# Kernel optimization log

Measured on AMD Instinct MI355X. Metric: run time of the kernel, lower is better.

The kernel has to match this reference:

```python
import jax, jax.numpy as jnp
import numpy as np
from functools import partial

K = 5
SCALE = 50000.0
OUT_CHN = 128
IN_CHN = 128
KS = 3

def setup_inputs() -> dict:
    key = jax.random.key(0)
    k1, k2, k3, k4, k5 = jax.random.split(key, 5)
    x = jax.random.normal(k1, (64, IN_CHN, 56, 56), dtype=jnp.float32)
    # xavier_normal-ish init for M and Z
    fan = IN_CHN * KS * KS + OUT_CHN * KS * KS
    std = float(np.sqrt(2.0 / fan))
    M = jax.random.normal(k2, (OUT_CHN, IN_CHN, KS, KS), dtype=jnp.float32) * std
    Z = jax.random.normal(k3, (K, OUT_CHN, IN_CHN, KS, KS), dtype=jnp.float32) * std
    Alpha = jax.random.uniform(k4, (OUT_CHN, 1, 1), dtype=jnp.float32)
    # rv ~ Normal(0, 1/sqrt(scale)), shape (1, K)
    rv = jax.random.normal(k5, (1, K), dtype=jnp.float32) / jnp.sqrt(jnp.float32(SCALE))
    return {"x": x, "M": M, "Z": Z, "Alpha": Alpha, "rv": rv}

def reference(x, M, Z, Alpha, rv):
    # --- SDP stochastic weight generation with pre-normalization ---
    m = M.reshape(-1)                      # (N,)
    z = Z.reshape(K, -1)                   # (K, N)
    A = m * m + jnp.sum(z * z, axis=0) / SCALE
    inv = jax.lax.rsqrt(A)
    m = m * inv
    z = z * inv
    w = (rv @ z)[0] + m                    # (N,)
    real_weights = w.reshape(OUT_CHN, IN_CHN, KS, KS)
    # --- binarize weights and activations ---
    bw = jnp.sign(real_weights)
    ba = jnp.sign(x)
    # --- conv2d, stride 1, padding 1, NCHW/OIHW ---
    out = jax.lax.conv_general_dilated(
        ba, bw, window_strides=(1, 1), padding=((1, 1), (1, 1)),
        dimension_numbers=("NCHW", "OIHW", "NCHW"))
    # per-output-channel scale Alpha (out,1,1) broadcasts over H,W
    out = out * Alpha[None]
    return out
```

## Files before the change

### kernel.cpp

```cpp
#include <hip/hip_runtime.h>
#include <stdint.h>

#define KK 5
#define SCALE_F 50000.0f
#define OC 128
#define IC 128
#define HH 56
#define WW 56
#define NB 64
#define HWSZ (HH * WW)
#define NTAP 9
#define NWEL (OC * IC * NTAP)

#define PD 58
#define NICQ 8

#define PW 60
#define PROWS 58
#define PLANE (PROWS * PW)
#define PLSTRIDE (NB * PLANE)
#define OCPB 2
#define WPT 4

typedef int v4i  __attribute__((ext_vector_type(4)));
typedef int v16i __attribute__((ext_vector_type(16)));

__device__ __forceinline__ constexpr int koff2(int kk) {
    int icb = kk / 9, tap = kk % 9;
    int dh = tap / 3 - 1, dw = tap % 3 - 1;
    return (dh * NICQ + icb * 2) * PD + dw;
}


__global__ void __launch_bounds__(256) border_kernel(int8_t* __restrict__ apk8) {
    int j = blockIdx.x * 256 + threadIdx.x;
    int n  = j / 1824;
    int rj = j - n * 1824;
    int hh, icq, ww;
    if (rj < 928) {
        hh = (rj / 464) * 57;
        int q = rj % 464;
        icq = q / PD;
        ww  = q - icq * PD;
    } else {
        int q = rj - 928;
        hh = 1 + (q >> 4);
        int r2 = q & 15;
        icq = r2 >> 1;
        ww  = (r2 & 1) * 57;
    }
    size_t chunk = (((size_t)n * PD + hh) * NICQ + icq) * PD + ww;
    *(int4*)(apk8 + chunk * 16) = make_int4(0, 0, 0, 0);
}

__global__ void __launch_bounds__(256) wpack_kernel(
    const float* __restrict__ M, const float* __restrict__ Z,
    const float* __restrict__ rv, int8_t* __restrict__ bfrag) {
    int i = blockIdx.x * 256 + threadIdx.x;
    int oc = i / 1152;
    int r1 = i - oc * 1152;
    int ic = r1 / 9;
    int tap = r1 - ic * 9;

    float m  = M[i];
    float z0 = Z[0 * NWEL + i];
    float z1 = Z[1 * NWEL + i];
    float z2 = Z[2 * NWEL + i];
    float z3 = Z[3 * NWEL + i];
    float z4 = Z[4 * NWEL + i];
    float s  = z0 * z0 + z1 * z1 + z2 * z2 + z3 * z3 + z4 * z4;
    float A  = m * m + s * (1.0f / SCALE_F);
    float inv = 1.0f / sqrtf(A);
    float w = rv[0] * (z0 * inv);
    w += rv[1] * (z1 * inv);
    w += rv[2] * (z2 * inv);
    w += rv[3] * (z3 * inv);
    w += rv[4] * (z4 * inv);
    w += m * inv;

    int8_t sv = (w > 0.0f) ? (int8_t)1 : (int8_t)-1;
    int icb = ic >> 5, khalf = (ic >> 4) & 1, b = ic & 15;
    int kk  = icb * 9 + tap;
    int oct = oc >> 5;
    int lane = khalf * 32 + (oc & 31);
    bfrag[(size_t)((kk * 4 + oct) * 64 + lane) * 16 + b] = sv;
}

__global__ void __launch_bounds__(448) apack_kernel(
    const float* __restrict__ x, int8_t* __restrict__ apk8) {
    int h = blockIdx.x;
    int n = blockIdx.y;
    int t = threadIdx.x;
    int w   = t % 56;
    int icq = t / 56;
    const float* xp = x + ((size_t)n * IC + icq * 16) * HWSZ + h * WW + w;

    uint32_t pk[4];
#pragma unroll
    for (int g = 0; g < 4; ++g) {
        uint32_t v = 0;
#pragma unroll
        for (int j = 0; j < 4; ++j) {
            float f = xp[(size_t)(g * 4 + j) * HWSZ];
            uint32_t sel = (f > 0.0f) ? 0x01u : 0xFFu;
            v |= sel << (8 * j);
        }
        pk[g] = v;
    }
    size_t chunk = (((size_t)n * PD + (h + 1)) * NICQ + icq) * PD + (w + 1);
    *(uint4*)(apk8 + chunk * 16) = make_uint4(pk[0], pk[1], pk[2], pk[3]);
}

__global__ void __launch_bounds__(768, 6) bconv_kernel(
    const int8_t* __restrict__ apk8, const int8_t* __restrict__ bfrag,
    const float* __restrict__ alpha, float* __restrict__ out) {
    __shared__ uint4 ldsB[4608];

    int tx = threadIdx.x;
    int lane = tx & 63, wid = tx >> 6;
    int half = lane >> 5, l31 = lane & 31;

    int bid = blockIdx.x;
    int xcd = bid & 7, pos = bid >> 3;
    int base = (xcd < 6) ? xcd * 131 : (6 * 131 + (xcd - 6) * 130);
    int swz = base + pos;
    int och = swz & 1;
    int pxb = swz >> 1;
    int ocb = och * 64;

    const uint4* gB = (const uint4*)bfrag;
#pragma unroll
    for (int s = 0; s < 6; ++s) {
        int idx = tx + s * 768;
        int kk = idx >> 7, j = (idx >> 6) & 1, ln = idx & 63;
        ldsB[idx] = gB[((kk << 2) + (och << 1) + j) * 64 + ln];
    }

    int px = pxb * 384 + wid * 32 + l31;
    int n  = px / HWSZ;
    int hw = px - n * HWSZ;
    int h  = hw / WW;
    int w  = hw - h * WW;
    int ab0 = ((n * PD + h + 1) * NICQ + half) * PD + (w + 1);
    size_t ob0 = ((size_t)n * OC + half) * HWSZ + hw;
    bool valid = (px < NB * HWSZ);

    __syncthreads();

    v16i acc0 = {}, acc1 = {};
    v4i a0 = *(const v4i*)(apk8 + ((size_t)(ab0 + koff2(0)) << 4));
    v4i a1 = *(const v4i*)(apk8 + ((size_t)(ab0 + koff2(1)) << 4));
    v4i a2 = *(const v4i*)(apk8 + ((size_t)(ab0 + koff2(2)) << 4));
    v4i a3;
    v4i b0c = *(const v4i*)&ldsB[0 * 128 + lane];
    v4i b1c = *(const v4i*)&ldsB[0 * 128 + 64 + lane];
    v4i b0n, b1n;

#pragma unroll
    for (int kk = 0; kk < 36; ++kk) {
        v4i A = (kk & 3) == 0 ? a0 : ((kk & 3) == 1 ? a1 : ((kk & 3) == 2 ? a2 : a3));
        if (kk + 3 < 36) {
            v4i t = *(const v4i*)(apk8 + ((size_t)(ab0 + koff2(kk + 3)) << 4));
            switch ((kk + 3) & 3) {
                case 0: a0 = t; break;
                case 1: a1 = t; break;
                case 2: a2 = t; break;
                default: a3 = t; break;
            }
        }
        if (kk + 1 < 36) {
            b0n = *(const v4i*)&ldsB[(kk + 1) * 128 + lane];
            b1n = *(const v4i*)&ldsB[(kk + 1) * 128 + 64 + lane];
        }
        acc0 = __builtin_amdgcn_mfma_i32_32x32x32_i8(A, b0c, acc0, 0, 0, 0);
        acc1 = __builtin_amdgcn_mfma_i32_32x32x32_i8(A, b1c, acc1, 0, 0, 0);
        b0c = b0n; b1c = b1n;
    }

    __syncthreads();

    float* tlw = (float*)ldsB + wid * (32 * 33);
    float alf[2];
    alf[0] = alpha[ocb + l31];
    alf[1] = alpha[ocb + 32 + l31];

#pragma unroll
    for (int tn = 0; tn < 2; ++tn) {
        const v16i* ac = tn ? &acc1 : &acc0;
#pragma unroll
        for (int r = 0; r < 16; ++r) {
            int row = (r & 3) + 8 * (r >> 2) + 4 * half;
            tlw[row * 33 + l31] = (float)(*ac)[r] * alf[tn];
        }
        if (valid) {
#pragma unroll
            for (int r = 0; r < 16; ++r) {
                float v = tlw[l31 * 33 + 2 * r + half];
                int oc = ocb + tn * 32 + 2 * r;
                out[ob0 + (size_t)oc * HWSZ] = v;
            }
        }
    }
}


__global__ void __launch_bounds__(256) wpack32_kernel(
    const float* __restrict__ M, const float* __restrict__ Z,
    const float* __restrict__ rv, uint32_t* __restrict__ wpk32) {
    int gtid = blockIdx.x * blockDim.x + threadIdx.x;
    int lane = gtid & 63;
    int wid  = gtid >> 6;
    int oc   = wid / 18;
    int r    = wid - oc * 18;
    int tap  = r >> 1;
    int word = r & 1;
    int ic   = word * 64 + lane;
    int idx  = (oc * IC + ic) * NTAP + tap;

    float m  = M[idx];
    float z0 = Z[0 * NWEL + idx];
    float z1 = Z[1 * NWEL + idx];
    float z2 = Z[2 * NWEL + idx];
    float z3 = Z[3 * NWEL + idx];
    float z4 = Z[4 * NWEL + idx];
    float s  = z0 * z0 + z1 * z1 + z2 * z2 + z3 * z3 + z4 * z4;
    float A  = m * m + s * (1.0f / SCALE_F);
    float inv = 1.0f / sqrtf(A);
    float w = rv[0] * (z0 * inv);
    w += rv[1] * (z1 * inv);
    w += rv[2] * (z2 * inv);
    w += rv[3] * (z3 * inv);
    w += rv[4] * (z4 * inv);
    w += m * inv;

    unsigned long long b = __ballot(w > 0.0f);
    if (lane == 0) {
        uint64_t* wpk = (uint64_t*)wpk32;
        wpk[(oc * NTAP + tap) * 2 + word] = b;
    }
}

__global__ void __launch_bounds__(256) apack32_kernel(
    const float* __restrict__ x, uint32_t* __restrict__ apk32) {
    int q  = blockIdx.x * blockDim.x + threadIdx.x;
    int wd = blockIdx.y;
    int n  = q / HWSZ;
    int hw = q - n * HWSZ;
    int h  = hw / WW;
    int w  = hw - h * WW;
    const float* xp = x + (size_t)n * IC * HWSZ + (size_t)wd * 32 * HWSZ + hw;

    uint32_t b = 0;
#pragma unroll
    for (int c = 0; c < 32; ++c)
        b |= (uint32_t)(xp[(size_t)c * HWSZ] > 0.0f) << c;

    apk32[(size_t)wd * PLSTRIDE + (size_t)n * PLANE + (size_t)(h + 1) * PW + (w + 1)] = b;
}

__global__ void __launch_bounds__(256, 8) bconv32_kernel(
    const uint32_t* __restrict__ apk32, const uint32_t* __restrict__ wpk32,
    const float* __restrict__ alpha, float* __restrict__ out) {
    __shared__ int adj[OCPB][9];
    __shared__ float alf[OCPB];

    int tx  = threadIdx.x;
    int oc0 = blockIdx.y * OCPB;

    if (tx < OCPB) alf[tx] = alpha[oc0 + tx];
    if (tx < OCPB * 9) {
        int ocl = tx / 9, cls = tx % 9;
        int rc = cls / 3, cc = cls % 3;
        int nv = ((rc == 1) ? 3 : 2) * ((cc == 1) ? 3 : 2);
        int s = 0;
#pragma unroll
        for (int t = 0; t < NTAP; ++t) {
            int i = t / 3, j = t % 3;
            bool invld = (rc == 0 && i == 0) || (rc == 2 && i == 2) ||
                         (cc == 0 && j == 0) || (cc == 2 && j == 2);
            if (invld) {
                const uint64_t* wpk = (const uint64_t*)wpk32;
                uint64_t lo = wpk[(oc0 + ocl) * NTAP * 2 + t * 2 + 0];
                uint64_t hi = wpk[(oc0 + ocl) * NTAP * 2 + t * 2 + 1];
                s += __popcll(lo) + __popcll(hi);
            }
        }
        adj[ocl][cls] = 128 * nv + 2 * s;
    }
    __syncthreads();

    int t  = blockIdx.x * blockDim.x + tx;
    int sw = t % 14;
    int h  = (t / 14) % HH;
    int n  = t / (14 * HH);
    int w0 = sw * WPT;

    const uint32_t* ap = apk32 + (size_t)n * PLANE + (size_t)h * PW + w0;
    const uint64_t* wpk = (const uint64_t*)wpk32;

    int cnt[WPT * OCPB] = {0};
#pragma unroll 1
    for (int r = 0; r < 3; ++r) {
#pragma unroll 1
        for (int wd = 0; wd < 4; ++wd) {
            const uint32_t* p = ap + (size_t)wd * PLSTRIDE + (size_t)r * PW;
            uint32_t T[6];
#pragma unroll
            for (int c = 0; c < 6; ++c) T[c] = p[c];
#pragma unroll
            for (int j = 0; j < 3; ++j) {
#pragma unroll
                for (int ocl = 0; ocl < OCPB; ++ocl) {
                    uint64_t w2 = wpk[(oc0 + ocl) * NTAP * 2 + (r * 3 + j) * 2 + (wd >> 1)];
                    uint32_t wv = (wd & 1) ? (uint32_t)(w2 >> 32) : (uint32_t)w2;
#pragma unroll
                    for (int o = 0; o < WPT; ++o)
                        cnt[o * OCPB + ocl] += __popc(T[j + o] ^ wv);
                }
            }
        }
    }

    int rcls = (h == 0) ? 0 : ((h == HH - 1) ? 6 : 3);
    int clsL = rcls + ((w0 == 0) ? 0 : 1);
    int clsI = rcls + 1;
    int clsR = rcls + ((w0 == WW - WPT) ? 2 : 1);
    float* op = out + ((size_t)n * OC + oc0) * HWSZ + h * WW + w0;
#pragma unroll
    for (int ocl = 0; ocl < OCPB; ++ocl) {
        float a = alf[ocl];
        float4 v;
        v.x = (float)(adj[ocl][clsL] - 2 * cnt[0 * OCPB + ocl]) * a;
        v.y = (float)(adj[ocl][clsI] - 2 * cnt[1 * OCPB + ocl]) * a;
        v.z = (float)(adj[ocl][clsI] - 2 * cnt[2 * OCPB + ocl]) * a;
        v.w = (float)(adj[ocl][clsR] - 2 * cnt[3 * OCPB + ocl]) * a;
        *(float4*)(op + (size_t)ocl * HWSZ) = v;
    }
}

extern "C" void kernel_launch(void* const* d_in, const int* in_sizes, int n_in,
                              void* d_out, int out_size, void* d_ws, size_t ws_size,
                              hipStream_t stream) {
    const float* x     = (const float*)d_in[0];
    const float* M     = (const float*)d_in[1];
    const float* Z     = (const float*)d_in[2];
    const float* Alpha = (const float*)d_in[3];
    const float* rv    = (const float*)d_in[4];
    float* out = (float*)d_out;

    const size_t mfma_needed = 196608 + (size_t)NB * PD * NICQ * PD * 16 + (1 << 20);

    if (ws_size >= mfma_needed) {
        int8_t* bfrag = (int8_t*)d_ws;
        int8_t* apk8  = (int8_t*)d_ws + 196608;

        border_kernel<<<(NB * 1824) / 256, 256, 0, stream>>>(apk8);
        wpack_kernel<<<NWEL / 256, 256, 0, stream>>>(M, Z, rv, bfrag);
        apack_kernel<<<dim3(HH, NB), 448, 0, stream>>>(x, apk8);
        bconv_kernel<<<1046, 768, 0, stream>>>(apk8, bfrag, Alpha, out);
    } else {
        uint32_t* wpk32 = (uint32_t*)d_ws;
        uint32_t* apk32 = (uint32_t*)((char*)d_ws + 32768);

        hipMemsetAsync(apk32, 0, (size_t)4 * PLSTRIDE * 4, stream);
        wpack32_kernel<<<NWEL / 256, 256, 0, stream>>>(M, Z, rv, wpk32);
        apack32_kernel<<<dim3((NB * HWSZ) / 256, 4), 256, 0, stream>>>(x, apk32);
        bconv32_kernel<<<dim3((NB * HH * 14) / 256, OC / OCPB), 256, 0, stream>>>(
            apk32, wpk32, Alpha, out);
    }
}
```

Measured before the change: 81.21 us.

## Shrink conv tile to one 32-channel output slice per wave and quadruple grid

The binary conv kernel now gives each block 256 pixels by 32 output channels (one MFMA accumulator per wave) instead of 384 pixels by 64 channels (two accumulators). The grid grows to 3136 blocks of 512 threads with a simpler XCD swizzle, LDS for weights halves, and the activation prefetch depth drops from 3 to 2. The bounds check disappears because pixels now divide evenly. This aims at higher occupancy and smaller per-block LDS, at the cost of loading each activation fragment once per 32 channels rather than once per 64, which doubles global activation traffic.

```diff
diff --git a/kernel.cpp b/kernel.cpp
--- a/kernel.cpp
+++ b/kernel.cpp
@@ -111,95 +111,75 @@
     *(uint4*)(apk8 + chunk * 16) = make_uint4(pk[0], pk[1], pk[2], pk[3]);
 }
 
-__global__ void __launch_bounds__(768, 6) bconv_kernel(
+__global__ void __launch_bounds__(512, 8) bconv_kernel(
     const int8_t* __restrict__ apk8, const int8_t* __restrict__ bfrag,
     const float* __restrict__ alpha, float* __restrict__ out) {
-    __shared__ uint4 ldsB[4608];
+    __shared__ uint4 ldsB[2304];
 
     int tx = threadIdx.x;
     int lane = tx & 63, wid = tx >> 6;
     int half = lane >> 5, l31 = lane & 31;
 
     int bid = blockIdx.x;
-    int xcd = bid & 7, pos = bid >> 3;
-    int base = (xcd < 6) ? xcd * 131 : (6 * 131 + (xcd - 6) * 130);
-    int swz = base + pos;
-    int och = swz & 1;
-    int pxb = swz >> 1;
-    int ocb = och * 64;
+    int swz = (bid & 7) * 392 + (bid >> 3);
+    int oq  = swz & 3;
+    int pxb = swz >> 2;
+    int ocb = oq * 32;
 
     const uint4* gB = (const uint4*)bfrag;
-#pragma unroll
-    for (int s = 0; s < 6; ++s) {
-        int idx = tx + s * 768;
-        int kk = idx >> 7, j = (idx >> 6) & 1, ln = idx & 63;
-        ldsB[idx] = gB[((kk << 2) + (och << 1) + j) * 64 + ln];
-    }
-
-    int px = pxb * 384 + wid * 32 + l31;
+    for (int idx = tx; idx < 2304; idx += 512) {
+        int kk = idx >> 6, ln = idx & 63;
+        ldsB[idx] = gB[((kk << 2) + oq) * 64 + ln];
+    }
+
+    int px = pxb * 256 + wid * 32 + l31;
     int n  = px / HWSZ;
     int hw = px - n * HWSZ;
     int h  = hw / WW;
     int w  = hw - h * WW;
     int ab0 = ((n * PD + h + 1) * NICQ + half) * PD + (w + 1);
-    size_t ob0 = ((size_t)n * OC + half) * HWSZ + hw;
-    bool valid = (px < NB * HWSZ);
+    size_t ob0 = ((size_t)n * OC + ocb + half) * HWSZ + hw;
 
     __syncthreads();
 
-    v16i acc0 = {}, acc1 = {};
+    v16i acc = {};
     v4i a0 = *(const v4i*)(apk8 + ((size_t)(ab0 + koff2(0)) << 4));
     v4i a1 = *(const v4i*)(apk8 + ((size_t)(ab0 + koff2(1)) << 4));
-    v4i a2 = *(const v4i*)(apk8 + ((size_t)(ab0 + koff2(2)) << 4));
-    v4i a3;
-    v4i b0c = *(const v4i*)&ldsB[0 * 128 + lane];
-    v4i b1c = *(const v4i*)&ldsB[0 * 128 + 64 + lane];
-    v4i b0n, b1n;
+    v4i a2;
+    v4i bc = *(const v4i*)&ldsB[0 * 64 + lane];
+    v4i bn;
 
 #pragma unroll
     for (int kk = 0; kk < 36; ++kk) {
-        v4i A = (kk & 3) == 0 ? a0 : ((kk & 3) == 1 ? a1 : ((kk & 3) == 2 ? a2 : a3));
-        if (kk + 3 < 36) {
-            v4i t = *(const v4i*)(apk8 + ((size_t)(ab0 + koff2(kk + 3)) << 4));
-            switch ((kk + 3) & 3) {
+        v4i A = (kk % 3) == 0 ? a0 : ((kk % 3) == 1 ? a1 : a2);
+        if (kk + 2 < 36) {
+            v4i t = *(const v4i*)(apk8 + ((size_t)(ab0 + koff2(kk + 2)) << 4));
+            switch ((kk + 2) % 3) {
                 case 0: a0 = t; break;
                 case 1: a1 = t; break;
-                case 2: a2 = t; break;
-                default: a3 = t; break;
+                default: a2 = t; break;
             }
         }
-        if (kk + 1 < 36) {
-            b0n = *(const v4i*)&ldsB[(kk + 1) * 128 + lane];
-            b1n = *(const v4i*)&ldsB[(kk + 1) * 128 + 64 + lane];
-        }
-        acc0 = __builtin_amdgcn_mfma_i32_32x32x32_i8(A, b0c, acc0, 0, 0, 0);
-        acc1 = __builtin_amdgcn_mfma_i32_32x32x32_i8(A, b1c, acc1, 0, 0, 0);
-        b0c = b0n; b1c = b1n;
+        if (kk + 1 < 36)
+            bn = *(const v4i*)&ldsB[(kk + 1) * 64 + lane];
+        acc = __builtin_amdgcn_mfma_i32_32x32x32_i8(A, bc, acc, 0, 0, 0);
+        bc = bn;
     }
 
     __syncthreads();
 
     float* tlw = (float*)ldsB + wid * (32 * 33);
-    float alf[2];
-    alf[0] = alpha[ocb + l31];
-    alf[1] = alpha[ocb + 32 + l31];
-
-#pragma unroll
-    for (int tn = 0; tn < 2; ++tn) {
-        const v16i* ac = tn ? &acc1 : &acc0;
-#pragma unroll
-        for (int r = 0; r < 16; ++r) {
-            int row = (r & 3) + 8 * (r >> 2) + 4 * half;
-            tlw[row * 33 + l31] = (float)(*ac)[r] * alf[tn];
-        }
-        if (valid) {
-#pragma unroll
-            for (int r = 0; r < 16; ++r) {
-                float v = tlw[l31 * 33 + 2 * r + half];
-                int oc = ocb + tn * 32 + 2 * r;
-                out[ob0 + (size_t)oc * HWSZ] = v;
-            }
-        }
+    float alf = alpha[ocb + l31];
+
+#pragma unroll
+    for (int r = 0; r < 16; ++r) {
+        int row = (r & 3) + 8 * (r >> 2) + 4 * half;
+        tlw[row * 33 + l31] = (float)acc[r] * alf;
+    }
+#pragma unroll
+    for (int r = 0; r < 16; ++r) {
+        float v = tlw[l31 * 33 + 2 * r + half];
+        out[ob0 + (size_t)(2 * r) * HWSZ] = v;
     }
 }
 
@@ -357,7 +337,7 @@
         border_kernel<<<(NB * 1824) / 256, 256, 0, stream>>>(apk8);
         wpack_kernel<<<NWEL / 256, 256, 0, stream>>>(M, Z, rv, bfrag);
         apack_kernel<<<dim3(HH, NB), 448, 0, stream>>>(x, apk8);
-        bconv_kernel<<<1046, 768, 0, stream>>>(apk8, bfrag, Alpha, out);
+        bconv_kernel<<<3136, 512, 0, stream>>>(apk8, bfrag, Alpha, out);
     } else {
         uint32_t* wpk32 = (uint32_t*)d_ws;
         uint32_t* apk32 = (uint32_t*)((char*)d_ws + 32768);
```

New measurement: 86.44 us. 1.06x slower.
